# Optimization experiments

Measured on AMD Instinct MI355X. Metric: run time of the kernel, lower is better.

Reference implementation:

```python
import jax, jax.numpy as jnp
import numpy as np

EMBED_DIM = 584  # module-global, used as softmax scale base (C ** -0.5)


def setup_inputs() -> dict:
    key = jax.random.key(0)
    ks = jax.random.split(key, 7)
    B, T, C, H, D = 16, 1024, 584, 8, 73
    x = jax.random.normal(ks[0], (B, T, C), dtype=jnp.float32)
    memory = jax.random.normal(ks[1], (B, T, C), dtype=jnp.float32)
    s = 0.02
    Wq = jax.random.normal(ks[2], (H, C, D), dtype=jnp.float32) * s
    Wk = jax.random.normal(ks[3], (H, C, D), dtype=jnp.float32) * s
    Wv = jax.random.normal(ks[4], (H, C, D), dtype=jnp.float32) * s
    Wp = jax.random.normal(ks[5], (C, C), dtype=jnp.float32) * s
    bp = jnp.zeros((C,), dtype=jnp.float32)
    return {"x": x, "memory": memory, "Wq": Wq, "Wk": Wk, "Wv": Wv, "Wp": Wp, "bp": bp}


def reference(x, memory, Wq, Wk, Wv, Wp, bp):
    B, T, C = x.shape
    # per-head projections, vectorized over heads: [B, H, T, D]
    q = jnp.einsum('btc,hcd->bhtd', x, Wq)
    k = jnp.einsum('bsc,hcd->bhsd', memory, Wk)
    v = jnp.einsum('btc,hcd->bhtd', x, Wv)  # NOTE: value from x, per original code
    # scale uses full embed dim C (not head size), per original code
    scores = jnp.einsum('bhtd,bhsd->bhts', q, k) * (C ** -0.5)
    weights = jax.nn.softmax(scores, axis=-1)
    # dropout is identity in eval/reference mode
    out = jnp.einsum('bhts,bhsd->bhtd', weights, v)  # requires S == T (matches original)
    out = out.transpose(0, 2, 1, 3).reshape(B, T, C)  # concat heads on last dim
    out = out @ Wp + bp  # output projection (dropout identity)
    return out
```

## Files before the change

### kernel.cpp

```cpp
#include <hip/hip_runtime.h>
#include <hip/hip_bf16.h>

typedef unsigned short u16;
typedef __attribute__((ext_vector_type(4))) unsigned short u16x4;
typedef __attribute__((ext_vector_type(8))) unsigned short u16x8;
typedef __attribute__((ext_vector_type(8))) __bf16 bf16x8;
typedef __attribute__((ext_vector_type(4))) float f32x4;

#define BB 16
#define TSEQ 1024
#define CC 584
#define HH 8
#define DHD 73
#define NR (BB*TSEQ)
#define KPW 640
#define DP 96
#define HD (HH*DP)
#define NP3 768
#define PPITCH 88
#define CEXP 0.0596985934f

__device__ __forceinline__ u16 f2bf(float f) {
  __bf16 h = (__bf16)f;
  return __builtin_bit_cast(u16, h);
}
__device__ __forceinline__ bf16x8 as_bf(u16x8 v) { return __builtin_bit_cast(bf16x8, v); }

#define GLL16(g, l) __builtin_amdgcn_global_load_lds( \
    (const __attribute__((address_space(1))) void*)(g), \
    (__attribute__((address_space(3))) void*)(l), 16, 0, 0)

#define BARRIER() asm volatile("s_barrier" ::: "memory")
#define LGKM0()   asm volatile("s_waitcnt lgkmcnt(0)" ::: "memory")
#define VMW4()    asm volatile("s_waitcnt vmcnt(4)" ::: "memory")
#define VMW2()    asm volatile("s_waitcnt vmcnt(2)" ::: "memory")
#define VMW0()    asm volatile("s_waitcnt vmcnt(0)" ::: "memory")

#define PKA 10240
#define PKB 5760
#define PKC 1920
__global__ void pack_all_kernel(const float* __restrict__ x, const float* __restrict__ mem,
                                const float* __restrict__ Wq, const float* __restrict__ Wk,
                                const float* __restrict__ Wv, const float* __restrict__ Wp,
                                u16* __restrict__ xmb, u16* __restrict__ wt,
                                u16* __restrict__ wpt) {
  const int bidx = blockIdx.x;
  const int tid = threadIdx.x;
  if (bidx < PKA) {
    int idx = bidx * 256 + tid;
    int row = idx / (KPW / 8);
    int c8  = (idx % (KPW / 8)) * 8;
    u16x8 o = {0, 0, 0, 0, 0, 0, 0, 0};
    if (c8 < CC) {
      const float* src = (row < NR) ? &x[(size_t)row * CC + c8]
                                    : &mem[(size_t)(row - NR) * CC + c8];
      f32x4 a = *(const f32x4*)src;
      f32x4 b = *(const f32x4*)(src + 4);
#pragma unroll
      for (int t = 0; t < 4; t++) { o[t] = f2bf(a[t]); o[4 + t] = f2bf(b[t]); }
    }
    *(u16x8*)&xmb[(size_t)row * KPW + c8] = o;
  } else if (bidx < PKA + PKB) {
    int idx = (bidx - PKA) * 256 + tid;
    int w   = idx / (HD * KPW);
    int rem = idx % (HD * KPW);
    int n = rem / KPW;
    int k = rem % KPW;
    int h = n / DP, d = n % DP;
    u16 val = 0;
    if (d < DHD && k < CC) {
      const float* W = (w == 0) ? Wq : ((w == 1) ? Wv : Wk);
      val = f2bf(W[((size_t)h * CC + k) * DHD + d]);
    }
    wt[idx] = val;
  } else {
    int idx = (bidx - PKA - PKB) * 256 + tid;
    int n = idx / KPW;
    int c = idx % KPW;
    u16 val = 0;
    if (n < CC && c < CC) val = f2bf(Wp[(size_t)c * CC + n]);
    wpt[idx] = val;
  }
}


template <int BUF, int MH>
__device__ __forceinline__ void rd_a(bf16x8 (&a)[4][2], const u16* lds, int arow,
                                     int sw0, int sw1) {
#pragma unroll
  for (int mq = 0; mq < 4; mq++) {
    const int r = BUF * 32768 + MH * 8192 + arow + mq * 1024;
    a[mq][0] = as_bf(*(const u16x8*)&lds[r + sw0]);
    a[mq][1] = as_bf(*(const u16x8*)&lds[r + sw1]);
  }
}
template <int BUF, int NH>
__device__ __forceinline__ void rd_b(bf16x8 (&b)[2][2], const u16* lds, int brow,
                                     int sw0, int sw1) {
#pragma unroll
  for (int nq = 0; nq < 2; nq++) {
    const int r = BUF * 32768 + 16384 + NH * 8192 + brow + nq * 1024;
    b[nq][0] = as_bf(*(const u16x8*)&lds[r + sw0]);
    b[nq][1] = as_bf(*(const u16x8*)&lds[r + sw1]);
  }
}
template <int BUF, int RG>
__device__ __forceinline__ void stg(const u16* gA, const u16* gB, u16* ldst, int t) {
  const u16* src = (RG < 2) ? gA : gB;
  const int rrow = (RG & 1) * 128;
  const int loff = BUF * 32768 + (RG >> 1) * 16384 + (RG & 1) * 8192;
  GLL16(src + (size_t)rrow * KPW + (size_t)t * 64, ldst + loff);
  GLL16(src + (size_t)(rrow + 64) * KPW + (size_t)t * 64, ldst + loff + 4096);
}
template <int MH, int NH>
__device__ __forceinline__ void mmq(f32x4 (&acc)[8][4], const bf16x8 (&a)[4][2],
                                    const bf16x8 (&b)[2][2]) {
  __builtin_amdgcn_s_setprio(1);
#pragma unroll
  for (int mq = 0; mq < 4; mq++)
#pragma unroll
    for (int nq = 0; nq < 2; nq++) {
      f32x4 c = acc[MH * 4 + mq][NH * 2 + nq];
      c = __builtin_amdgcn_mfma_f32_16x16x32_bf16(a[mq][0], b[nq][0], c, 0, 0, 0);
      c = __builtin_amdgcn_mfma_f32_16x16x32_bf16(a[mq][1], b[nq][1], c, 0, 0, 0);
      acc[MH * 4 + mq][NH * 2 + nq] = c;
    }
  __builtin_amdgcn_s_setprio(0);
}

template <int MODE>
__global__ __launch_bounds__(512, 2) void gemm8_kernel(
    const u16* __restrict__ A, const u16* __restrict__ Bt,
    void* __restrict__ CoutV, void* __restrict__ CoutV2,
    const float* __restrict__ bias) {
  extern __shared__ u16 lds[];
  const int tid  = threadIdx.x;
  const int lane = tid & 63;
  const int q15  = lane & 15;
  const int quad = lane >> 4;
  const int wave = tid >> 6;
  const int wmi  = wave >> 2;
  const int wni  = wave & 3;

  const int cpx = gridDim.x >> 3;
  const int bid = (blockIdx.x & 7) * cpx + (blockIdx.x >> 3);

  int m0, n0, npart;
  if (MODE == 4) {
    if (bid < 384) {
      m0 = (bid / 6) * 256; int nt = bid % 6;
      n0 = nt * 256; npart = (nt >= 3) ? 1 : 0;
    } else {
      int b2 = bid - 384;
      m0 = NR + (b2 / 3) * 256; n0 = 1536 + (b2 % 3) * 256; npart = 2;
    }
  } else {
    m0 = (bid / 3) * 256; n0 = (bid % 3) * 256; npart = 0;
  }

  const int tr   = tid >> 3;
  const int scol = ((tid & 7) ^ (tr & 7)) * 8;
  const u16* gA = &A[(size_t)(m0 + tr) * KPW + scol];
  const u16* gB = &Bt[(size_t)(n0 + tr) * KPW + scol];
  u16* ldst = &lds[tid * 8];

  const int rb  = q15 & 7;
  const int sw0 = (quad ^ rb) * 8;
  const int sw1 = ((quad + 4) ^ rb) * 8;
  const int arow = (wmi * 64 + q15) * 64;
  const int brow = (wni * 32 + q15) * 64;

  f32x4 acc[8][4];
#pragma unroll
  for (int i = 0; i < 8; i++)
#pragma unroll
    for (int j = 0; j < 4; j++) acc[i][j] = (f32x4){0.f, 0.f, 0.f, 0.f};
  bf16x8 a[4][2], b0[2][2], b1[2][2];

  stg<0, 0>(gA, gB, ldst, 0);
  stg<0, 2>(gA, gB, ldst, 0);
  stg<0, 3>(gA, gB, ldst, 0);
  stg<0, 1>(gA, gB, ldst, 0);
  VMW4(); BARRIER();

#pragma unroll 1
  for (int i = 0; i < 5; ++i) {
    const int t1 = 2 * i + 1;
    const int t2 = 2 * i + 2;
    const bool st = (i < 4);
    rd_a<0, 0>(a, lds, arow, sw0, sw1);
    rd_b<0, 0>(b0, lds, brow, sw0, sw1);
    stg<1, 0>(gA, gB, ldst, t1);
    VMW4(); BARRIER(); LGKM0();
    mmq<0, 0>(acc, a, b0);
    BARRIER();
    rd_b<0, 1>(b1, lds, brow, sw0, sw1);
    stg<1, 2>(gA, gB, ldst, t1);
    VMW4(); BARRIER(); LGKM0();
    mmq<0, 1>(acc, a, b1);
    BARRIER();
    rd_a<0, 1>(a, lds, arow, sw0, sw1);
    stg<1, 3>(gA, gB, ldst, t1);
    VMW4(); BARRIER(); LGKM0();
    mmq<1, 0>(acc, a, b0);
    BARRIER();
    stg<1, 1>(gA, gB, ldst, t1);
    VMW4(); BARRIER();
    mmq<1, 1>(acc, a, b1);
    BARRIER();
    rd_a<1, 0>(a, lds, arow, sw0, sw1);
    rd_b<1, 0>(b0, lds, brow, sw0, sw1);
    if (st) { stg<0, 0>(gA, gB, ldst, t2); VMW4(); } else { VMW2(); }
    BARRIER(); LGKM0();
    mmq<0, 0>(acc, a, b0);
    BARRIER();
    rd_b<1, 1>(b1, lds, brow, sw0, sw1);
    if (st) { stg<0, 2>(gA, gB, ldst, t2); VMW4(); } else { VMW0(); }
    BARRIER(); LGKM0();
    mmq<0, 1>(acc, a, b1);
    BARRIER();
    rd_a<1, 1>(a, lds, arow, sw0, sw1);
    if (st) { stg<0, 3>(gA, gB, ldst, t2); VMW4(); }
    BARRIER(); LGKM0();
    mmq<1, 0>(acc, a, b0);
    BARRIER();
    if (st) { stg<0, 1>(gA, gB, ldst, t2); VMW4(); }
    BARRIER();
    mmq<1, 1>(acc, a, b1);
    BARRIER();
  }

  const int rowb = m0 + wmi * 64 + quad * 4;
  const int colb = n0 + wni * 32 + q15;
#pragma unroll
  for (int mh = 0; mh < 2; mh++)
#pragma unroll
    for (int mq = 0; mq < 4; mq++)
#pragma unroll
      for (int nh = 0; nh < 2; nh++)
#pragma unroll
        for (int nq = 0; nq < 2; nq++) {
          const f32x4 av = acc[mh * 4 + mq][nh * 2 + nq];
          const int row = rowb + mh * 128 + mq * 16;
          const int col = colb + nh * 128 + nq * 16;
          if (MODE == 4) {
            if (npart == 2) {
              u16* Cout = (u16*)CoutV2;
              const int rk = row - NR;
              const int ck = col - 1536;
#pragma unroll
              for (int r = 0; r < 4; r++)
                Cout[(size_t)(rk + r) * HD + ck] = f2bf(av[r]);
            } else if (npart == 0) {
              u16* Cout = (u16*)CoutV;
#pragma unroll
              for (int r = 0; r < 4; r++)
                Cout[(size_t)(row + r) * HD + col] = f2bf(av[r]);
            } else {
              u16* Cout = (u16*)CoutV;
              const int vn = col - HD;
              const int bb = row >> 10;
              const int tl = row & 1023;
              u16x4 pk;
#pragma unroll
              for (int r = 0; r < 4; r++) pk[r] = f2bf(av[r]);
              *(u16x4*)&Cout[(size_t)(NR * HD) + ((size_t)(bb * HD + vn)) * TSEQ + tl] = pk;
            }
          } else {
            if (col < CC) {
              float* Cout = (float*)CoutV;
              const float bvv = bias[col];
#pragma unroll
              for (int r = 0; r < 4; r++)
                Cout[(size_t)(row + r) * CC + col] = av[r] + bvv;
            }
          }
        }
}

__global__ __launch_bounds__(256, 3) void attn_kernel(
    const u16* __restrict__ qb, const u16* __restrict__ kb,
    const u16* __restrict__ vt, u16* __restrict__ attn) {
  __shared__ u16 smem[128 * 96 + 64 * 104 + 96 * 72];
  u16* Qs = smem;
  u16* Ks = smem + 128 * 96;
  u16* Vs = smem + 128 * 96 + 64 * 104;
  u16* Pt = smem;

  const int tid  = threadIdx.x;
  const int lane = tid & 63;
  const int wave = tid >> 6;
  const int q15  = lane & 15;
  const int quad = lane >> 4;
  const int bid  = blockIdx.x;
  const int loc  = bid >> 3;
  const int pair = (bid & 7) * 16 + (loc >> 3);
  const int b  = pair >> 3;
  const int h  = pair & 7;
  const int t0 = (loc & 7) * 128;
  const int wq0 = wave * 32;

  int krow[3], kc[3], vrow[3], vc[3];
#pragma unroll
  for (int p = 0; p < 3; p++) {
    int qk = tid + 256 * p;
    krow[p] = qk / 12; kc[p] = (qk % 12) * 8;
    int qv = tid + 256 * p;
    vrow[p] = qv / 8;  vc[p] = (qv % 8) * 8;
  }
  const u16* kbase = &kb[(size_t)(b * TSEQ) * HD + h * DP];
  const u16* vbase = &vt[(size_t)(b * HD + h * DP) * TSEQ];

  for (int q = tid; q < 128 * 12; q += 256) {
    int row = q / 12, c8 = (q % 12) * 8;
    *(u16x8*)&Qs[row * 96 + c8] =
        *(const u16x8*)&qb[(size_t)(b * TSEQ + t0 + row) * HD + h * DP + c8];
  }
  if (tid < 128) {
    const u16x8 z = {0, 0, 0, 0, 0, 0, 0, 0};
    size_t base = (size_t)(b * TSEQ + t0 + tid) * KPW + CC;
#pragma unroll
    for (int c = 0; c < (KPW - CC) / 8; c++) *(u16x8*)&attn[base + c * 8] = z;
  }
  __syncthreads();

  bf16x8 aq[2][3];
#pragma unroll
  for (int n = 0; n < 2; n++)
#pragma unroll
    for (int kcx = 0; kcx < 3; kcx++)
      aq[n][kcx] = as_bf(*(const u16x8*)&Qs[(wq0 + n * 16 + q15) * 96 + kcx * 32 + quad * 8]);

  float lsum[2] = {0.f, 0.f};
  f32x4 oacc[2][6];
#pragma unroll
  for (int m = 0; m < 2; m++)
#pragma unroll
    for (int jd = 0; jd < 6; jd++) oacc[m][jd] = (f32x4){0.f, 0.f, 0.f, 0.f};

  u16* Ptw = &Pt[wave * 32 * PPITCH];

  u16x8 kreg[3], vreg[3];
#pragma unroll
  for (int p = 0; p < 3; p++) {
    kreg[p] = *(const u16x8*)&kbase[(size_t)krow[p] * HD + kc[p]];
    vreg[p] = *(const u16x8*)&vbase[(size_t)vrow[p] * TSEQ + vc[p]];
  }

  for (int si = 0; si < 16; ++si) {
#pragma unroll
    for (int p = 0; p < 3; p++) {
      *(u16x8*)&Ks[krow[p] * 104 + kc[p]] = kreg[p];
      *(u16x8*)&Vs[vrow[p] * 72 + vc[p]]  = vreg[p];
    }
    __syncthreads();

    if (si < 15) {
      const int s1 = (si + 1) * 64;
#pragma unroll
      for (int p = 0; p < 3; p++) {
        kreg[p] = *(const u16x8*)&kbase[(size_t)(s1 + krow[p]) * HD + kc[p]];
        vreg[p] = *(const u16x8*)&vbase[(size_t)vrow[p] * TSEQ + s1 + vc[p]];
      }
    }

    f32x4 st[4][2];
#pragma unroll
    for (int mt = 0; mt < 4; mt++)
#pragma unroll
      for (int n = 0; n < 2; n++) st[mt][n] = (f32x4){0.f, 0.f, 0.f, 0.f};
#pragma unroll
    for (int kcx = 0; kcx < 3; kcx++) {
      bf16x8 ak[4];
#pragma unroll
      for (int mt = 0; mt < 4; mt++)
        ak[mt] = as_bf(*(const u16x8*)&Ks[(mt * 16 + q15) * 104 + kcx * 32 + quad * 8]);
#pragma unroll
      for (int mt = 0; mt < 4; mt++)
#pragma unroll
        for (int n = 0; n < 2; n++)
          st[mt][n] = __builtin_amdgcn_mfma_f32_16x16x32_bf16(ak[mt], aq[n][kcx], st[mt][n], 0, 0, 0);
    }

#pragma unroll
    for (int mt = 0; mt < 4; mt++)
#pragma unroll
      for (int n = 0; n < 2; n++) {
        f32x4 pv;
#pragma unroll
        for (int r = 0; r < 4; r++) pv[r] = __builtin_amdgcn_exp2f(st[mt][n][r] * CEXP);
        lsum[n] += (pv[0] + pv[1]) + (pv[2] + pv[3]);
        u16x4 pk;
#pragma unroll
        for (int r = 0; r < 4; r++) pk[r] = f2bf(pv[r]);
        *(u16x4*)&Ptw[(n * 16 + q15) * PPITCH + mt * 16 + quad * 4] = pk;
      }

#pragma unroll
    for (int kcx = 0; kcx < 2; kcx++) {
      bf16x8 ap[2];
#pragma unroll
      for (int m = 0; m < 2; m++)
        ap[m] = as_bf(*(const u16x8*)&Ptw[(m * 16 + q15) * PPITCH + kcx * 32 + quad * 8]);
#pragma unroll
      for (int jd = 0; jd < 6; jd++) {
        bf16x8 bv = as_bf(*(const u16x8*)&Vs[(jd * 16 + q15) * 72 + kcx * 32 + quad * 8]);
#pragma unroll
        for (int m = 0; m < 2; m++)
          oacc[m][jd] = __builtin_amdgcn_mfma_f32_16x16x32_bf16(ap[m], bv, oacc[m][jd], 0, 0, 0);
      }
    }
    __syncthreads();
  }

  float lr[2];
#pragma unroll
  for (int n = 0; n < 2; n++) {
    float s = lsum[n];
    s += __shfl_xor(s, 16);
    s += __shfl_xor(s, 32);
    lr[n] = s;
  }

#pragma unroll
  for (int m = 0; m < 2; m++) {
#pragma unroll
    for (int r = 0; r < 4; r++) {
      const float inv = 1.f / __shfl(lr[m], quad * 4 + r);
      const int trow = t0 + wq0 + m * 16 + quad * 4 + r;
#pragma unroll
      for (int jd = 0; jd < 5; jd++) {
        const int d = jd * 16 + q15;
        if (d < DHD)
          attn[(size_t)(b * TSEQ + trow) * KPW + h * DHD + d] = f2bf(oacc[m][jd][r] * inv);
      }
    }
  }
}


extern "C" void kernel_launch(void* const* d_in, const int* in_sizes, int n_in,
                              void* d_out, int out_size, void* d_ws, size_t ws_size,
                              hipStream_t stream) {
  const float* x   = (const float*)d_in[0];
  const float* mem = (const float*)d_in[1];
  const float* Wq  = (const float*)d_in[2];
  const float* Wk  = (const float*)d_in[3];
  const float* Wv  = (const float*)d_in[4];
  const float* Wp  = (const float*)d_in[5];
  const float* bp  = (const float*)d_in[6];
  float* out = (float*)d_out;

  char* ws = (char*)d_ws;
  const size_t SZ_XMB = (size_t)2 * NR * KPW * 2;
  const size_t SZ_WT  = (size_t)3 * HD * KPW * 2;
  const size_t SZ_WPT = (size_t)NP3 * KPW * 2;
  const size_t SZ_QB  = (size_t)NR * HD * 2;

  u16* xmb    = (u16*)(ws);
  u16* attn_o = (u16*)(ws);
  u16* wt     = (u16*)(ws + SZ_XMB);
  u16* wp_t   = (u16*)(ws + SZ_XMB + SZ_WT);
  u16* q_buf  = (u16*)(ws + SZ_XMB + SZ_WT + SZ_WPT);
  u16* vt_buf = q_buf + (size_t)NR * HD;
  u16* k_buf  = (u16*)(ws + SZ_XMB + SZ_WT + SZ_WPT + 2 * SZ_QB);

  (void)in_sizes; (void)n_in; (void)out_size; (void)ws_size;

  static bool s_attr = false;
  if (!s_attr) {
    (void)hipFuncSetAttribute((const void*)gemm8_kernel<4>,
                              hipFuncAttributeMaxDynamicSharedMemorySize, 131072);
    (void)hipFuncSetAttribute((const void*)gemm8_kernel<2>,
                              hipFuncAttributeMaxDynamicSharedMemorySize, 131072);
    s_attr = true;
  }

  pack_all_kernel<<<PKA + PKB + PKC, 256, 0, stream>>>(x, mem, Wq, Wk, Wv, Wp,
                                                       xmb, wt, wp_t);

  gemm8_kernel<4><<<576, 512, 131072, stream>>>(xmb, wt, q_buf, k_buf, nullptr);

  attn_kernel<<<BB * HH * (TSEQ / 128), 256, 0, stream>>>(q_buf, k_buf, vt_buf, attn_o);

  gemm8_kernel<2><<<192, 512, 131072, stream>>>(attn_o, wp_t, out, nullptr, bp);
}
```

Baseline: 291.8 us.

## Deepen GEMM prefetch pipeline, coarsen weight packing, raise MFMA priority in attention

The GEMM main loop now issues global-to-LDS stages two at a time and keeps more loads in flight, waiting on vmcnt(8) instead of vmcnt(4). This is meant to hide more memory latency behind MFMA work. The weight-packing blocks each process 8 elements per thread, which cuts the block count by a factor of 8. In the attention kernel, s_setprio wraps the MFMA sections so waves issuing matrix ops get priority. The deeper prefetch relies on the vmcnt counts matching the buffer reuse pattern, and a wrong count could cause a race.

```diff
diff --git a/kernel.cpp b/kernel.cpp
--- a/kernel.cpp
+++ b/kernel.cpp
@@ -32,13 +32,13 @@
 
 #define BARRIER() asm volatile("s_barrier" ::: "memory")
 #define LGKM0()   asm volatile("s_waitcnt lgkmcnt(0)" ::: "memory")
+#define VMW8()    asm volatile("s_waitcnt vmcnt(8)" ::: "memory")
 #define VMW4()    asm volatile("s_waitcnt vmcnt(4)" ::: "memory")
-#define VMW2()    asm volatile("s_waitcnt vmcnt(2)" ::: "memory")
 #define VMW0()    asm volatile("s_waitcnt vmcnt(0)" ::: "memory")
 
 #define PKA 10240
-#define PKB 5760
-#define PKC 1920
+#define PKB2 720
+#define PKC2 240
 __global__ void pack_all_kernel(const float* __restrict__ x, const float* __restrict__ mem,
                                 const float* __restrict__ Wq, const float* __restrict__ Wk,
                                 const float* __restrict__ Wv, const float* __restrict__ Wp,
@@ -60,26 +60,34 @@
       for (int t = 0; t < 4; t++) { o[t] = f2bf(a[t]); o[4 + t] = f2bf(b[t]); }
     }
     *(u16x8*)&xmb[(size_t)row * KPW + c8] = o;
-  } else if (bidx < PKA + PKB) {
-    int idx = (bidx - PKA) * 256 + tid;
-    int w   = idx / (HD * KPW);
-    int rem = idx % (HD * KPW);
-    int n = rem / KPW;
-    int k = rem % KPW;
-    int h = n / DP, d = n % DP;
-    u16 val = 0;
-    if (d < DHD && k < CC) {
-      const float* W = (w == 0) ? Wq : ((w == 1) ? Wv : Wk);
-      val = f2bf(W[((size_t)h * CC + k) * DHD + d]);
-    }
-    wt[idx] = val;
+  } else if (bidx < PKA + PKB2) {
+    const int base = (bidx - PKA) * 2048 + tid;
+#pragma unroll
+    for (int e = 0; e < 8; e++) {
+      int idx = base + e * 256;
+      int w   = idx / (HD * KPW);
+      int rem = idx % (HD * KPW);
+      int n = rem / KPW;
+      int k = rem % KPW;
+      int h = n / DP, d = n % DP;
+      u16 val = 0;
+      if (d < DHD && k < CC) {
+        const float* W = (w == 0) ? Wq : ((w == 1) ? Wv : Wk);
+        val = f2bf(W[((size_t)h * CC + k) * DHD + d]);
+      }
+      wt[idx] = val;
+    }
   } else {
-    int idx = (bidx - PKA - PKB) * 256 + tid;
-    int n = idx / KPW;
-    int c = idx % KPW;
-    u16 val = 0;
-    if (n < CC && c < CC) val = f2bf(Wp[(size_t)c * CC + n]);
-    wpt[idx] = val;
+    const int base = (bidx - PKA - PKB2) * 2048 + tid;
+#pragma unroll
+    for (int e = 0; e < 8; e++) {
+      int idx = base + e * 256;
+      int n = idx / KPW;
+      int c = idx % KPW;
+      u16 val = 0;
+      if (n < CC && c < CC) val = f2bf(Wp[(size_t)c * CC + n]);
+      wpt[idx] = val;
+    }
   }
 }
 
@@ -181,50 +189,52 @@
   stg<0, 2>(gA, gB, ldst, 0);
   stg<0, 3>(gA, gB, ldst, 0);
   stg<0, 1>(gA, gB, ldst, 0);
-  VMW4(); BARRIER();
+  stg<1, 0>(gA, gB, ldst, 1);
+  stg<1, 2>(gA, gB, ldst, 1);
+  VMW8(); BARRIER();
 
 #pragma unroll 1
   for (int i = 0; i < 5; ++i) {
     const int t1 = 2 * i + 1;
     const int t2 = 2 * i + 2;
+    const int t3 = 2 * i + 3;
     const bool st = (i < 4);
     rd_a<0, 0>(a, lds, arow, sw0, sw1);
     rd_b<0, 0>(b0, lds, brow, sw0, sw1);
-    stg<1, 0>(gA, gB, ldst, t1);
-    VMW4(); BARRIER(); LGKM0();
+    stg<1, 3>(gA, gB, ldst, t1);
+    stg<1, 1>(gA, gB, ldst, t1);
+    VMW8(); BARRIER(); LGKM0();
     mmq<0, 0>(acc, a, b0);
     BARRIER();
     rd_b<0, 1>(b1, lds, brow, sw0, sw1);
-    stg<1, 2>(gA, gB, ldst, t1);
-    VMW4(); BARRIER(); LGKM0();
+    BARRIER(); LGKM0();
     mmq<0, 1>(acc, a, b1);
     BARRIER();
     rd_a<0, 1>(a, lds, arow, sw0, sw1);
-    stg<1, 3>(gA, gB, ldst, t1);
-    VMW4(); BARRIER(); LGKM0();
+    BARRIER(); LGKM0();
     mmq<1, 0>(acc, a, b0);
     BARRIER();
-    stg<1, 1>(gA, gB, ldst, t1);
-    VMW4(); BARRIER();
+    if (st) { stg<0, 0>(gA, gB, ldst, t2); stg<0, 2>(gA, gB, ldst, t2); VMW8(); }
+    else { VMW4(); }
+    BARRIER();
     mmq<1, 1>(acc, a, b1);
     BARRIER();
     rd_a<1, 0>(a, lds, arow, sw0, sw1);
     rd_b<1, 0>(b0, lds, brow, sw0, sw1);
-    if (st) { stg<0, 0>(gA, gB, ldst, t2); VMW4(); } else { VMW2(); }
+    if (st) { stg<0, 3>(gA, gB, ldst, t2); stg<0, 1>(gA, gB, ldst, t2); VMW8(); }
+    else { VMW0(); }
     BARRIER(); LGKM0();
     mmq<0, 0>(acc, a, b0);
     BARRIER();
     rd_b<1, 1>(b1, lds, brow, sw0, sw1);
-    if (st) { stg<0, 2>(gA, gB, ldst, t2); VMW4(); } else { VMW0(); }
     BARRIER(); LGKM0();
     mmq<0, 1>(acc, a, b1);
     BARRIER();
     rd_a<1, 1>(a, lds, arow, sw0, sw1);
-    if (st) { stg<0, 3>(gA, gB, ldst, t2); VMW4(); }
     BARRIER(); LGKM0();
     mmq<1, 0>(acc, a, b0);
     BARRIER();
-    if (st) { stg<0, 1>(gA, gB, ldst, t2); VMW4(); }
+    if (st) { stg<1, 0>(gA, gB, ldst, t3); stg<1, 2>(gA, gB, ldst, t3); VMW8(); }
     BARRIER();
     mmq<1, 1>(acc, a, b1);
     BARRIER();
@@ -369,6 +379,7 @@
     for (int mt = 0; mt < 4; mt++)
 #pragma unroll
       for (int n = 0; n < 2; n++) st[mt][n] = (f32x4){0.f, 0.f, 0.f, 0.f};
+    __builtin_amdgcn_s_setprio(1);
 #pragma unroll
     for (int kcx = 0; kcx < 3; kcx++) {
       bf16x8 ak[4];
@@ -381,6 +392,7 @@
         for (int n = 0; n < 2; n++)
           st[mt][n] = __builtin_amdgcn_mfma_f32_16x16x32_bf16(ak[mt], aq[n][kcx], st[mt][n], 0, 0, 0);
     }
+    __builtin_amdgcn_s_setprio(0);
 
 #pragma unroll
     for (int mt = 0; mt < 4; mt++)
@@ -396,6 +408,7 @@
         *(u16x4*)&Ptw[(n * 16 + q15) * PPITCH + mt * 16 + quad * 4] = pk;
       }
 
+    __builtin_amdgcn_s_setprio(1);
 #pragma unroll
     for (int kcx = 0; kcx < 2; kcx++) {
       bf16x8 ap[2];
@@ -410,6 +423,7 @@
           oacc[m][jd] = __builtin_amdgcn_mfma_f32_16x16x32_bf16(ap[m], bv, oacc[m][jd], 0, 0, 0);
       }
     }
+    __builtin_amdgcn_s_setprio(0);
     __syncthreads();
   }
 
@@ -476,8 +490,8 @@
     s_attr = true;
   }
 
-  pack_all_kernel<<<PKA + PKB + PKC, 256, 0, stream>>>(x, mem, Wq, Wk, Wv, Wp,
-                                                       xmb, wt, wp_t);
+  pack_all_kernel<<<PKA + PKB2 + PKC2, 256, 0, stream>>>(x, mem, Wq, Wk, Wv, Wp,
+                                                         xmb, wt, wp_t);
 
   gemm8_kernel<4><<<576, 512, 131072, stream>>>(xmb, wt, q_buf, k_buf, nullptr);
 
```

Result: slower. 301.9 us (+3.5%).
